# Kernel tuning notes

Measured on AMD Instinct MI355X. Metric: run time of the kernel, lower is better.

Reference implementation:

```python
import jax, jax.numpy as jnp
import numpy as np

BN_EPS = 1e-5
B, N, D, E, L, VOCAB = 256, 256, 256, 262144, 5, 16
V = B * N


def batch_norm(h, g, b):
    # BatchNorm1d in training mode: biased batch stats over the node axis
    mu = jnp.mean(h, axis=0)
    var = jnp.mean((h - mu) ** 2, axis=0)
    return (h - mu) * jax.lax.rsqrt(var + BN_EPS) * g + b


def setup_inputs() -> dict:
    key = jax.random.key(0)
    ks = jax.random.split(key, 10)
    return {
        "x": jax.random.normal(ks[0], (B, N + 1, D), jnp.float32),
        "edge_weight": jax.random.uniform(ks[1], (E,), jnp.float32),
        "bond_emb": 0.02 * jax.random.normal(ks[2], (L, 3, VOCAB, D), jnp.float32),
        "W1": 0.02 * jax.random.normal(ks[3], (L, D, 2 * D), jnp.float32),
        "b1": jnp.zeros((L, 2 * D), jnp.float32),
        "bn1_g": jnp.ones((L, 2 * D), jnp.float32),
        "bn1_b": jnp.zeros((L, 2 * D), jnp.float32),
        "W2": 0.02 * jax.random.normal(ks[4], (L, 2 * D, D), jnp.float32),
        "b2": jnp.zeros((L, D), jnp.float32),
        "bn2_g": jnp.ones((L, D), jnp.float32),
        "bn2_b": jnp.zeros((L, D), jnp.float32),
        "eps_param": jnp.zeros((L,), jnp.float32),
        "x_mask": jnp.ones((B, N), jnp.int32),
        "edge_index": jax.random.randint(ks[5], (2, E), 0, V, jnp.int32),
        "edge_attr": jax.random.randint(ks[6], (E, 3), 0, VOCAB, jnp.int32),
    }


def reference(x, edge_weight, bond_emb, W1, b1, bn1_g, bn1_b, W2, b2,
              bn2_g, bn2_b, eps_param, x_mask, edge_index, edge_attr):
    res = x
    # mask is all-ones -> x[x_mask] equals the flattened [B*N, D] node tensor
    h = x[:, 1:, :].reshape(-1, D)
    mask = x_mask.reshape(-1).astype(x.dtype)[:, None]

    # add_self_loops: append (i, i) for every node; self-loop attr = [5, 7, 0]
    sl = jnp.arange(V, dtype=edge_index.dtype)
    src = jnp.concatenate([edge_index[0], sl])
    dst = jnp.concatenate([edge_index[1], sl])
    ea = jnp.concatenate(
        [edge_attr, jnp.broadcast_to(jnp.array([5, 7, 0], edge_attr.dtype), (V, 3))], axis=0)
    ew = jnp.concatenate([edge_weight, jnp.ones((V,), edge_weight.dtype)])

    for i in range(L):
        # BondEncoder: sum of per-feature embedding lookups -> [E+V, D]
        eemb = (bond_emb[i, 0][ea[:, 0]] + bond_emb[i, 1][ea[:, 1]]
                + bond_emb[i, 2][ea[:, 2]])
        msg = jax.nn.relu(h[src] + eemb) * ew[:, None]       # gather + relu
        aggr = jax.ops.segment_sum(msg, dst, num_segments=V)  # scatter-add
        z = (1.0 + eps_param[i]) * h + aggr
        z = batch_norm(z @ W1[i] + b1[i], bn1_g[i], bn1_b[i])
        z = jax.nn.relu(z) @ W2[i] + b2[i]
        z = batch_norm(z, bn2_g[i], bn2_b[i])                 # GNNBlock norm
        if i != L - 1:                                        # last_act
            z = jax.nn.relu(z)
        h = z                                                  # drop_ratio=0

    rep = h * mask  # x_zeros[x_mask] = node_representation (JK='last')
    return res.at[:, 1:, :].add(rep.reshape(res.shape[0], -1, D))
```

## Files before the change

kernel.cpp:

```cpp
#include <hip/hip_runtime.h>

#define E_EDGES 262144
#define V_NODES 65536
#define D_DIM   256

typedef short bf16x8 __attribute__((ext_vector_type(8)));
typedef float f32x4  __attribute__((ext_vector_type(4)));

__device__ __forceinline__ unsigned short f2bf(float f) {
  union { float f; unsigned u; } x; x.f = f;
  unsigned r = x.u + 0x7FFFu + ((x.u >> 16) & 1u);
  return (unsigned short)(r >> 16);
}
__device__ __forceinline__ float bf2f(unsigned short h) {
  union { unsigned u; float f; } x; x.u = ((unsigned)h) << 16;
  return x.f;
}
__device__ __forceinline__ void async16(const void* g, void* l) {
  __builtin_amdgcn_global_load_lds(
      (const __attribute__((address_space(1))) unsigned*)g,
      (__attribute__((address_space(3))) unsigned*)l, 16, 0, 0);
}

__global__ __launch_bounds__(256) void convert_weights_kernel(
    const float* __restrict__ W1, const float* __restrict__ W2,
    unsigned short* __restrict__ W1T, unsigned short* __restrict__ W2T) {
  int idx = blockIdx.x * 256 + threadIdx.x;
  {
    int k = idx & 255, n = (idx >> 8) & 511, i = idx >> 17;
    W1T[idx] = f2bf(W1[((size_t)(i * 256 + k)) * 512 + n]);
  }
  {
    int k = idx & 511, n = (idx >> 9) & 255, i = idx >> 17;
    W2T[idx] = f2bf(W2[((size_t)(i * 512 + k)) * 256 + n]);
  }
}

__global__ void hist_kernel(const int* __restrict__ ei, int* __restrict__ counts) {
  int e = blockIdx.x * 256 + threadIdx.x;
  int d = (e < E_EDGES) ? ei[E_EDGES + e] : (e - E_EDGES);
  atomicAdd(&counts[d], 1);
}
__global__ void scan1_kernel(const int* __restrict__ counts, int* __restrict__ indptr,
                             int* __restrict__ bsums) {
  __shared__ int s[256];
  int t = threadIdx.x, b = blockIdx.x;
  int v = counts[b * 256 + t];
  s[t] = v; __syncthreads();
  for (int off = 1; off < 256; off <<= 1) {
    int add = (t >= off) ? s[t - off] : 0;
    __syncthreads();
    s[t] += add;
    __syncthreads();
  }
  indptr[b * 256 + t] = s[t] - v;
  if (t == 255) bsums[b] = s[255];
}
__global__ void scan2_kernel(const int* __restrict__ bsums, int* __restrict__ boff) {
  __shared__ int s[256];
  int t = threadIdx.x;
  int v = bsums[t];
  s[t] = v; __syncthreads();
  for (int off = 1; off < 256; off <<= 1) {
    int add = (t >= off) ? s[t - off] : 0;
    __syncthreads();
    s[t] += add;
    __syncthreads();
  }
  boff[t] = s[t] - v;
}
__global__ void scan3_kernel(int* __restrict__ indptr, const int* __restrict__ boff) {
  int t = threadIdx.x, b = blockIdx.x;
  indptr[b * 256 + t] += boff[b];
  if (b == 0 && t == 0) indptr[V_NODES] = E_EDGES + V_NODES;
}
__global__ void scatter_kernel(const int* __restrict__ ei, const int* __restrict__ indptr,
                               int* __restrict__ fill, int* __restrict__ csr_eid) {
  int e = blockIdx.x * 256 + threadIdx.x;
  int d = (e < E_EDGES) ? ei[E_EDGES + e] : (e - E_EDGES);
  int pos = indptr[d] + atomicAdd(&fill[d], 1);
  csr_eid[pos] = e;
}

template <bool L0>
__device__ __forceinline__ void load_hnorm(int node, int c0, const float* __restrict__ x,
                                           const unsigned short* __restrict__ hprev,
                                           const float* sc, const float* sh, float* out) {
  if (L0) {
    const float* p = x + ((size_t)((node >> 8) * 257 + (node & 255) + 1)) * 256 + c0;
    float4 tv = *(const float4*)p;
    out[0] = tv.x; out[1] = tv.y; out[2] = tv.z; out[3] = tv.w;
  } else {
    ushort4 tv = *(const ushort4*)(hprev + (size_t)node * 256 + c0);
    out[0] = fmaxf(bf2f(tv.x) * sc[0] + sh[0], 0.f);
    out[1] = fmaxf(bf2f(tv.y) * sc[1] + sh[1], 0.f);
    out[2] = fmaxf(bf2f(tv.z) * sc[2] + sh[2], 0.f);
    out[3] = fmaxf(bf2f(tv.w) * sc[3] + sh[3], 0.f);
  }
}

template <bool L0>
__global__ __launch_bounds__(256) void msg_kernel(
    const float* __restrict__ x, const unsigned short* __restrict__ hprev,
    const float* __restrict__ scale2, const float* __restrict__ shift2,
    const int* __restrict__ indptr, const int* __restrict__ csr_eid,
    const int* __restrict__ ei, const int* __restrict__ ea, const float* __restrict__ ew,
    const float* __restrict__ bemb, const float* __restrict__ eps_param, int layer,
    float* __restrict__ aggr_f) {
  int wid = threadIdx.x >> 6;
  int lane = threadIdx.x & 63;
  int v = blockIdx.x * 4 + wid;
  int c0 = lane * 4;
  float ep = 1.0f + eps_param[layer];

  float sc[4], sh[4];
  if (!L0) {
#pragma unroll
    for (int j = 0; j < 4; ++j) { sc[j] = scale2[c0 + j]; sh[j] = shift2[c0 + j]; }
  }

  float hv[4];
  load_hnorm<L0>(v, c0, x, hprev, sc, sh, hv);
  float acc[4] = { ep * hv[0], ep * hv[1], ep * hv[2], ep * hv[3] };

  int beg = indptr[v], end = indptr[v + 1];
  int eid = csr_eid[beg];
  int s, a0, a1, a2; float w;
  if (eid < E_EDGES) {
    s = ei[eid]; a0 = ea[eid * 3]; a1 = ea[eid * 3 + 1]; a2 = ea[eid * 3 + 2]; w = ew[eid];
  } else { s = eid - E_EDGES; a0 = 5; a1 = 7; a2 = 0; w = 1.0f; }

  for (int p = beg; p < end; ++p) {
    float hs[4];
    load_hnorm<L0>(s, c0, x, hprev, sc, sh, hs);
    float4 e0 = *(const float4*)(bemb + (size_t)(a0) * 256 + c0);
    float4 e1 = *(const float4*)(bemb + (size_t)(16 + a1) * 256 + c0);
    float4 e2 = *(const float4*)(bemb + (size_t)(32 + a2) * 256 + c0);
    float wc = w;

    if (p + 1 < end) {
      int eidn = csr_eid[p + 1];
      if (eidn < E_EDGES) {
        s = ei[eidn]; a0 = ea[eidn * 3]; a1 = ea[eidn * 3 + 1]; a2 = ea[eidn * 3 + 2];
        w = ew[eidn];
      } else { s = eidn - E_EDGES; a0 = 5; a1 = 7; a2 = 0; w = 1.0f; }
    }

    acc[0] += fmaxf(hs[0] + e0.x + e1.x + e2.x, 0.f) * wc;
    acc[1] += fmaxf(hs[1] + e0.y + e1.y + e2.y, 0.f) * wc;
    acc[2] += fmaxf(hs[2] + e0.z + e1.z + e2.z, 0.f) * wc;
    acc[3] += fmaxf(hs[3] + e0.w + e1.w + e2.w, 0.f) * wc;
  }
  float4 o; o.x = acc[0]; o.y = acc[1]; o.z = acc[2]; o.w = acc[3];
  *(float4*)(aggr_f + (size_t)v * 256 + c0) = o;
}

__global__ __launch_bounds__(256) void colsum_kernel(const float* __restrict__ aggr_f,
                                                     float* __restrict__ colsum) {
  int t = threadIdx.x;
  size_t base = (size_t)blockIdx.x * 64 * 256 + t;
  float s = 0.f;
#pragma unroll
  for (int r = 0; r < 64; ++r) s += aggr_f[base + (size_t)r * 256];
  atomicAdd(&colsum[t], s);
}

__global__ __launch_bounds__(256) void center_kernel(const float* __restrict__ aggr_f,
                                                     const float* __restrict__ colsum,
                                                     unsigned short* __restrict__ aggr_c) {
  size_t i = ((size_t)blockIdx.x * 256 + threadIdx.x) * 4;
  int c = (int)(i & 255);
  float4 v = *(const float4*)(aggr_f + i);
  const float inv = 1.0f / 65536.0f;
  ushort4 o;
  o.x = f2bf(v.x - colsum[c + 0] * inv);
  o.y = f2bf(v.y - colsum[c + 1] * inv);
  o.z = f2bf(v.z - colsum[c + 2] * inv);
  o.w = f2bf(v.w - colsum[c + 3] * inv);
  *(ushort4*)(aggr_c + i) = o;
}

template <int K, int N>
__global__ __launch_bounds__(256) void gemm_kernel(
    const unsigned short* __restrict__ A, const unsigned short* __restrict__ BT,
    const float* __restrict__ bias, unsigned short* __restrict__ C,
    float* __restrict__ sumP, float* __restrict__ sqP) {
  __shared__ char lds[16384];
  const int t = threadIdx.x;
  const int lane = t & 63;
  const int wid = t >> 6;
  const int waveM = wid >> 1, waveN = wid & 1;
  const int rowBase = blockIdx.x * 128;
  const int colBase = blockIdx.y * 128;
  const int kw = lane >> 4;
  const int l15 = lane & 15;

  f32x4 acc[4][4];
#pragma unroll
  for (int m = 0; m < 4; ++m)
#pragma unroll
    for (int n = 0; n < 4; ++n) acc[m][n] = (f32x4){0.f, 0.f, 0.f, 0.f};

  for (int k0 = 0; k0 < K; k0 += 32) {
#pragma unroll
    for (int c = 0; c < 2; ++c) {
      int row = c * 64 + (t >> 2);
      int gslot = (t & 3) ^ ((row >> 1) & 3);
      const unsigned short* ga = A + (size_t)(rowBase + row) * K + k0 + gslot * 8;
      async16(ga, lds + c * 4096 + wid * 1024);
      const unsigned short* gb = BT + (size_t)(colBase + row) * K + k0 + gslot * 8;
      async16(gb, lds + 8192 + c * 4096 + wid * 1024);
    }
    __syncthreads();

    bf16x8 af[4], bfr[4];
#pragma unroll
    for (int f = 0; f < 4; ++f) {
      int rA = waveM * 64 + f * 16 + l15;
      af[f] = *(const bf16x8*)(lds + rA * 64 + ((kw ^ ((rA >> 1) & 3)) * 16));
      int rB = waveN * 64 + f * 16 + l15;
      bfr[f] = *(const bf16x8*)(lds + 8192 + rB * 64 + ((kw ^ ((rB >> 1) & 3)) * 16));
    }
#pragma unroll
    for (int m = 0; m < 4; ++m)
#pragma unroll
      for (int n = 0; n < 4; ++n)
        acc[m][n] = __builtin_amdgcn_mfma_f32_16x16x32_bf16(af[m], bfr[n], acc[m][n], 0, 0, 0);
    __syncthreads();
  }

  const int cB = colBase + waveN * 64;
  const int rB0 = rowBase + waveM * 64;
#pragma unroll
  for (int n = 0; n < 4; ++n) {
    int col = cB + n * 16 + l15;
    float bcol = bias[col];
    float psum = 0.f, psq = 0.f;
#pragma unroll
    for (int m = 0; m < 4; ++m) {
#pragma unroll
      for (int r = 0; r < 4; ++r) {
        float val = acc[m][n][r] + bcol;
        int row = rB0 + m * 16 + kw * 4 + r;
        C[(size_t)row * N + col] = f2bf(val);
        psum += val; psq += val * val;
      }
    }
    psum += __shfl_xor(psum, 16); psum += __shfl_xor(psum, 32);
    psq  += __shfl_xor(psq, 16);  psq  += __shfl_xor(psq, 32);
    if (kw == 0) {
      int prow = blockIdx.x * 2 + waveM;
      sumP[(size_t)prow * N + col] = psum;
      sqP[(size_t)prow * N + col] = psq;
    }
  }
}

__global__ __launch_bounds__(256) void gemm2_kernel(
    const unsigned short* __restrict__ A , const unsigned short* __restrict__ BT,
    const float* __restrict__ scA, const float* __restrict__ shA,
    const float* __restrict__ bias, float* __restrict__ C ,
    float* __restrict__ sumP, float* __restrict__ sqP) {
  const int K = 512, N = 256;
  __shared__ char lds[16384];
  const int t = threadIdx.x;
  const int lane = t & 63;
  const int wid = t >> 6;
  const int waveM = wid >> 1, waveN = wid & 1;
  const int rowBase = blockIdx.x * 128;
  const int colBase = blockIdx.y * 128;
  const int kw = lane >> 4;
  const int l15 = lane & 15;

  f32x4 acc[4][4];
#pragma unroll
  for (int m = 0; m < 4; ++m)
#pragma unroll
    for (int n = 0; n < 4; ++n) acc[m][n] = (f32x4){0.f, 0.f, 0.f, 0.f};

  for (int k0 = 0; k0 < K; k0 += 32) {
#pragma unroll
    for (int c = 0; c < 2; ++c) {
      int row = c * 64 + (t >> 2);
      int gslot = (t & 3) ^ ((row >> 1) & 3);
      const unsigned short* gb = BT + (size_t)(colBase + row) * K + k0 + gslot * 8;
      async16(gb, lds + 8192 + c * 4096 + wid * 1024);
    }
#pragma unroll
    for (int c = 0; c < 2; ++c) {
      int row = c * 64 + (t >> 2);
      int gslot = (t & 3) ^ ((row >> 1) & 3);
      int kk = k0 + gslot * 8;
      const unsigned short* ga = A + (size_t)(rowBase + row) * K + kk;
      ushort4 a0 = *(const ushort4*)ga;
      ushort4 a1 = *(const ushort4*)(ga + 4);
      float4 s0 = *(const float4*)(scA + kk);
      float4 s1 = *(const float4*)(scA + kk + 4);
      float4 h0 = *(const float4*)(shA + kk);
      float4 h1 = *(const float4*)(shA + kk + 4);
      bf16x8 o;
      o[0] = (short)f2bf(fmaxf(bf2f(a0.x) * s0.x + h0.x, 0.f));
      o[1] = (short)f2bf(fmaxf(bf2f(a0.y) * s0.y + h0.y, 0.f));
      o[2] = (short)f2bf(fmaxf(bf2f(a0.z) * s0.z + h0.z, 0.f));
      o[3] = (short)f2bf(fmaxf(bf2f(a0.w) * s0.w + h0.w, 0.f));
      o[4] = (short)f2bf(fmaxf(bf2f(a1.x) * s1.x + h1.x, 0.f));
      o[5] = (short)f2bf(fmaxf(bf2f(a1.y) * s1.y + h1.y, 0.f));
      o[6] = (short)f2bf(fmaxf(bf2f(a1.z) * s1.z + h1.z, 0.f));
      o[7] = (short)f2bf(fmaxf(bf2f(a1.w) * s1.w + h1.w, 0.f));
      *(bf16x8*)(lds + c * 4096 + wid * 1024 + (t & 63) * 16) = o;
    }
    __syncthreads();

    bf16x8 af[4], bfr[4];
#pragma unroll
    for (int f = 0; f < 4; ++f) {
      int rA = waveM * 64 + f * 16 + l15;
      af[f] = *(const bf16x8*)(lds + rA * 64 + ((kw ^ ((rA >> 1) & 3)) * 16));
      int rB = waveN * 64 + f * 16 + l15;
      bfr[f] = *(const bf16x8*)(lds + 8192 + rB * 64 + ((kw ^ ((rB >> 1) & 3)) * 16));
    }
#pragma unroll
    for (int m = 0; m < 4; ++m)
#pragma unroll
      for (int n = 0; n < 4; ++n)
        acc[m][n] = __builtin_amdgcn_mfma_f32_16x16x32_bf16(af[m], bfr[n], acc[m][n], 0, 0, 0);
    __syncthreads();
  }

  const int cB = colBase + waveN * 64;
  const int rB0 = rowBase + waveM * 64;
#pragma unroll
  for (int n = 0; n < 4; ++n) {
    int col = cB + n * 16 + l15;
    float bcol = bias[col];
    float psum = 0.f, psq = 0.f;
#pragma unroll
    for (int m = 0; m < 4; ++m) {
#pragma unroll
      for (int r = 0; r < 4; ++r) {
        float val = acc[m][n][r] + bcol;
        int row = rB0 + m * 16 + kw * 4 + r;
        C[(size_t)row * N + col] = val;
        psum += val; psq += val * val;
      }
    }
    psum += __shfl_xor(psum, 16); psum += __shfl_xor(psum, 32);
    psq  += __shfl_xor(psq, 16);  psq  += __shfl_xor(psq, 32);
    if (kw == 0) {
      int prow = blockIdx.x * 2 + waveM;
      sumP[(size_t)prow * N + col] = psum;
      sqP[(size_t)prow * N + col] = psq;
    }
  }
}

__global__ void finalize_kernel(const float* __restrict__ sumP, const float* __restrict__ sqP,
                                const float* __restrict__ g, const float* __restrict__ b,
                                float* __restrict__ scale, float* __restrict__ shift, int N) {
  __shared__ float ls[256], lq[256];
  int col = blockIdx.x, t = threadIdx.x;
  float s = 0.f, q = 0.f;
  for (int r = t; r < 1024; r += 256) {
    s += sumP[(size_t)r * N + col];
    q += sqP[(size_t)r * N + col];
  }
  ls[t] = s; lq[t] = q; __syncthreads();
  for (int off = 128; off > 0; off >>= 1) {
    if (t < off) { ls[t] += ls[t + off]; lq[t] += lq[t + off]; }
    __syncthreads();
  }
  if (t == 0) {
    float inv = 1.0f / 65536.0f;
    float mu = ls[0] * inv;
    float var = lq[0] * inv - mu * mu;
    float sc = g[col] * rsqrtf(var + 1e-5f);
    scale[col] = sc;
    shift[col] = b[col] - mu * sc;
  }
}

__global__ void finalize2_kernel(const float* __restrict__ sumP, const float* __restrict__ sqP,
                                 const float* __restrict__ g, const float* __restrict__ b,
                                 float* __restrict__ scale, float* __restrict__ shift,
                                 float* __restrict__ mu_out, int N) {
  __shared__ float ls[256], lq[256];
  int col = blockIdx.x, t = threadIdx.x;
  float s = 0.f, q = 0.f;
  for (int r = t; r < 1024; r += 256) {
    s += sumP[(size_t)r * N + col];
    q += sqP[(size_t)r * N + col];
  }
  ls[t] = s; lq[t] = q; __syncthreads();
  for (int off = 128; off > 0; off >>= 1) {
    if (t < off) { ls[t] += ls[t + off]; lq[t] += lq[t + off]; }
    __syncthreads();
  }
  if (t == 0) {
    float inv = 1.0f / 65536.0f;
    float mu = ls[0] * inv;
    float var = lq[0] * inv - mu * mu;
    scale[col] = g[col] * rsqrtf(var + 1e-5f);
    shift[col] = b[col];
    mu_out[col] = mu;
  }
}

__global__ __launch_bounds__(256) void center2_kernel(const float* __restrict__ z2f,
                                                      const float* __restrict__ mu2,
                                                      unsigned short* __restrict__ z2c) {
  size_t i = ((size_t)blockIdx.x * 256 + threadIdx.x) * 4;
  int c = (int)(i & 255);
  float4 v = *(const float4*)(z2f + i);
  ushort4 o;
  o.x = f2bf(v.x - mu2[c + 0]);
  o.y = f2bf(v.y - mu2[c + 1]);
  o.z = f2bf(v.z - mu2[c + 2]);
  o.w = f2bf(v.w - mu2[c + 3]);
  *(ushort4*)(z2c + i) = o;
}

__global__ void final_out_kernel(const float* __restrict__ x, const unsigned short* __restrict__ z2c,
                                 const float* __restrict__ scale2, const float* __restrict__ shift2,
                                 const int* __restrict__ xmask, float* __restrict__ out) {
  int row = blockIdx.x;
  int b = blockIdx.y;
  int lane = threadIdx.x;
  size_t off = ((size_t)b * 257 + row) * 256 + lane * 4;
  float4 xv = *(const float4*)(x + off);
  if (row > 0) {
    int v = b * 256 + (row - 1);
    float m = (float)xmask[v];
    ushort4 tv = *(const ushort4*)(z2c + (size_t)v * 256 + lane * 4);
    int c = lane * 4;
    xv.x += m * (bf2f(tv.x) * scale2[c + 0] + shift2[c + 0]);
    xv.y += m * (bf2f(tv.y) * scale2[c + 1] + shift2[c + 1]);
    xv.z += m * (bf2f(tv.z) * scale2[c + 2] + shift2[c + 2]);
    xv.w += m * (bf2f(tv.w) * scale2[c + 3] + shift2[c + 3]);
  }
  *(float4*)(out + off) = xv;
}

extern "C" void kernel_launch(void* const* d_in, const int* in_sizes, int n_in,
                              void* d_out, int out_size, void* d_ws, size_t ws_size,
                              hipStream_t stream) {
  const float* x    = (const float*)d_in[0];
  const float* ew   = (const float*)d_in[1];
  const float* bemb = (const float*)d_in[2];
  const float* W1   = (const float*)d_in[3];
  const float* b1   = (const float*)d_in[4];
  const float* g1   = (const float*)d_in[5];
  const float* bb1  = (const float*)d_in[6];
  const float* W2   = (const float*)d_in[7];
  const float* b2   = (const float*)d_in[8];
  const float* g2   = (const float*)d_in[9];
  const float* bb2  = (const float*)d_in[10];
  const float* eps  = (const float*)d_in[11];
  const int* xmask  = (const int*)d_in[12];
  const int* ei     = (const int*)d_in[13];
  const int* ea     = (const int*)d_in[14];
  float* out = (float*)d_out;

  char* ws = (char*)d_ws;
  size_t off = 0;
  auto alloc = [&](size_t bytes) {
    char* p = ws + off;
    off += (bytes + 255) & ~(size_t)255;
    return p;
  };
  unsigned short* W1T = (unsigned short*)alloc(5ull * 512 * 256 * 2);
  unsigned short* W2T = (unsigned short*)alloc(5ull * 256 * 512 * 2);
  int* counts = (int*)alloc(65536ull * 4);
  int* fill   = (int*)alloc(65536ull * 4);
  int* indptr = (int*)alloc(65537ull * 4);
  int* bsums  = (int*)alloc(256 * 4);
  int* boff   = (int*)alloc(256 * 4);
  int* csr    = (int*)alloc(327680ull * 4);
  float* scale1 = (float*)alloc(512 * 4);
  float* shift1 = (float*)alloc(512 * 4);
  float* scale2 = (float*)alloc(256 * 4);
  float* shift2 = (float*)alloc(256 * 4);
  float* colsum = (float*)alloc(256 * 4);
  float* mu2    = (float*)alloc(256 * 4);
  float* sumP = (float*)alloc(1024ull * 512 * 4);
  float* sqP  = (float*)alloc(1024ull * 512 * 4);
  float* aggr_f = (float*)alloc(65536ull * 256 * 4);
  unsigned short* aggr_c = (unsigned short*)alloc(65536ull * 256 * 2);
  unsigned short* z1   = (unsigned short*)alloc(65536ull * 512 * 2);
  unsigned short* z2c  = (unsigned short*)alloc(65536ull * 256 * 2);
  (void)ws_size; (void)in_sizes; (void)n_in; (void)out_size;

  hipMemsetAsync(counts, 0, 65536ull * 4, stream);
  hipMemsetAsync(fill, 0, 65536ull * 4, stream);

  convert_weights_kernel<<<2560, 256, 0, stream>>>(W1, W2, W1T, W2T);
  hist_kernel<<<1280, 256, 0, stream>>>(ei, counts);
  scan1_kernel<<<256, 256, 0, stream>>>(counts, indptr, bsums);
  scan2_kernel<<<1, 256, 0, stream>>>(bsums, boff);
  scan3_kernel<<<256, 256, 0, stream>>>(indptr, boff);
  scatter_kernel<<<1280, 256, 0, stream>>>(ei, indptr, fill, csr);

  for (int i = 0; i < 5; ++i) {
    const float* bemb_l = bemb + (size_t)i * 3 * 16 * 256;
    if (i == 0)
      msg_kernel<true><<<16384, 256, 0, stream>>>(x, (const unsigned short*)nullptr, nullptr, nullptr,
                                                  indptr, csr, ei, ea, ew, bemb_l, eps, i, aggr_f);
    else
      msg_kernel<false><<<16384, 256, 0, stream>>>(x, z2c, scale2, shift2,
                                                   indptr, csr, ei, ea, ew, bemb_l, eps, i, aggr_f);
    hipMemsetAsync(colsum, 0, 256 * 4, stream);
    colsum_kernel<<<1024, 256, 0, stream>>>(aggr_f, colsum);
    center_kernel<<<16384, 256, 0, stream>>>(aggr_f, colsum, aggr_c);
    gemm_kernel<256, 512><<<dim3(512, 4), 256, 0, stream>>>(
        aggr_c, W1T + (size_t)i * 512 * 256, b1 + i * 512, z1, sumP, sqP);
    finalize_kernel<<<512, 256, 0, stream>>>(sumP, sqP, g1 + i * 512, bb1 + i * 512,
                                             scale1, shift1, 512);
    gemm2_kernel<<<dim3(512, 2), 256, 0, stream>>>(
        z1, W2T + (size_t)i * 256 * 512, scale1, shift1, b2 + i * 256, aggr_f, sumP, sqP);
    finalize2_kernel<<<256, 256, 0, stream>>>(sumP, sqP, g2 + i * 256, bb2 + i * 256,
                                              scale2, shift2, mu2, 256);
    center2_kernel<<<16384, 256, 0, stream>>>(aggr_f, mu2, z2c);
  }
  final_out_kernel<<<dim3(257, 256), 64, 0, stream>>>(x, z2c, scale2, shift2, xmask, out);
}
```

Measured before the change: 1.458 ms.

## Fuse centering into GEMM1 A-load, prefetch full edge data, skip last center2

The separate center kernel is removed. GEMM1 now reads fp32 aggregates directly, subtracts the column mean, converts to bf16 and writes the result into LDS, which avoids a full bf16 round trip through memory per layer. The message kernel now issues the next edge's feature and embedding loads one iteration ahead for deeper prefetch. The last layer also skips center2, and the final output is computed from the fp32 buffer. The cost is that GEMM1's A-tile path loses async global-to-LDS loads, so it reads twice the bytes and spends VALU work on the conversion.

```diff
diff --git a/kernel.cpp b/kernel.cpp
--- a/kernel.cpp
+++ b/kernel.cpp
@@ -83,20 +83,37 @@
 }
 
 template <bool L0>
-__device__ __forceinline__ void load_hnorm(int node, int c0, const float* __restrict__ x,
-                                           const unsigned short* __restrict__ hprev,
-                                           const float* sc, const float* sh, float* out) {
+struct EdgeBuf {
+  float4 hrawf;
+  ushort4 hrawb;
+  float4 e0, e1, e2;
+  float w;
+};
+
+template <bool L0>
+__device__ __forceinline__ void resolve_and_issue(
+    int p, int c0, const int* __restrict__ csr_eid, const int* __restrict__ ei,
+    const int* __restrict__ ea, const float* __restrict__ ew,
+    const float* __restrict__ x, const unsigned short* __restrict__ hprev,
+    const float* __restrict__ bemb, EdgeBuf<L0>& B) {
+  int eid = csr_eid[p];
+  int s, a0, a1, a2;
+  if (eid < E_EDGES) {
+    s = ei[eid];
+    a0 = ea[eid * 3]; a1 = ea[eid * 3 + 1]; a2 = ea[eid * 3 + 2];
+    B.w = ew[eid];
+  } else {
+    s = eid - E_EDGES; a0 = 5; a1 = 7; a2 = 0; B.w = 1.0f;
+  }
   if (L0) {
-    const float* p = x + ((size_t)((node >> 8) * 257 + (node & 255) + 1)) * 256 + c0;
-    float4 tv = *(const float4*)p;
-    out[0] = tv.x; out[1] = tv.y; out[2] = tv.z; out[3] = tv.w;
+    const float* pp = x + ((size_t)((s >> 8) * 257 + (s & 255) + 1)) * 256 + c0;
+    B.hrawf = *(const float4*)pp;
   } else {
-    ushort4 tv = *(const ushort4*)(hprev + (size_t)node * 256 + c0);
-    out[0] = fmaxf(bf2f(tv.x) * sc[0] + sh[0], 0.f);
-    out[1] = fmaxf(bf2f(tv.y) * sc[1] + sh[1], 0.f);
-    out[2] = fmaxf(bf2f(tv.z) * sc[2] + sh[2], 0.f);
-    out[3] = fmaxf(bf2f(tv.w) * sc[3] + sh[3], 0.f);
-  }
+    B.hrawb = *(const ushort4*)(hprev + (size_t)s * 256 + c0);
+  }
+  B.e0 = *(const float4*)(bemb + (size_t)(a0) * 256 + c0);
+  B.e1 = *(const float4*)(bemb + (size_t)(16 + a1) * 256 + c0);
+  B.e2 = *(const float4*)(bemb + (size_t)(32 + a2) * 256 + c0);
 }
 
 template <bool L0>
@@ -120,38 +137,49 @@
   }
 
   float hv[4];
-  load_hnorm<L0>(v, c0, x, hprev, sc, sh, hv);
-  float acc[4] = { ep * hv[0], ep * hv[1], ep * hv[2], ep * hv[3] };
+  if (L0) {
+    const float* p = x + ((size_t)((v >> 8) * 257 + (v & 255) + 1)) * 256 + c0;
+    float4 tv = *(const float4*)p;
+    hv[0] = tv.x; hv[1] = tv.y; hv[2] = tv.z; hv[3] = tv.w;
+  } else {
+    ushort4 tv = *(const ushort4*)(hprev + (size_t)v * 256 + c0);
+    hv[0] = fmaxf(bf2f(tv.x) * sc[0] + sh[0], 0.f);
+    hv[1] = fmaxf(bf2f(tv.y) * sc[1] + sh[1], 0.f);
+    hv[2] = fmaxf(bf2f(tv.z) * sc[2] + sh[2], 0.f);
+    hv[3] = fmaxf(bf2f(tv.w) * sc[3] + sh[3], 0.f);
+  }
+
+  float acc[4] = { 0.f, 0.f, 0.f, 0.f };
 
   int beg = indptr[v], end = indptr[v + 1];
-  int eid = csr_eid[beg];
-  int s, a0, a1, a2; float w;
-  if (eid < E_EDGES) {
-    s = ei[eid]; a0 = ea[eid * 3]; a1 = ea[eid * 3 + 1]; a2 = ea[eid * 3 + 2]; w = ew[eid];
-  } else { s = eid - E_EDGES; a0 = 5; a1 = 7; a2 = 0; w = 1.0f; }
+  EdgeBuf<L0> cur, nxt;
+  resolve_and_issue<L0>(beg, c0, csr_eid, ei, ea, ew, x, hprev, bemb, cur);
 
   for (int p = beg; p < end; ++p) {
+    if (p + 1 < end)
+      resolve_and_issue<L0>(p + 1, c0, csr_eid, ei, ea, ew, x, hprev, bemb, nxt);
+
     float hs[4];
-    load_hnorm<L0>(s, c0, x, hprev, sc, sh, hs);
-    float4 e0 = *(const float4*)(bemb + (size_t)(a0) * 256 + c0);
-    float4 e1 = *(const float4*)(bemb + (size_t)(16 + a1) * 256 + c0);
-    float4 e2 = *(const float4*)(bemb + (size_t)(32 + a2) * 256 + c0);
-    float wc = w;
-
-    if (p + 1 < end) {
-      int eidn = csr_eid[p + 1];
-      if (eidn < E_EDGES) {
-        s = ei[eidn]; a0 = ea[eidn * 3]; a1 = ea[eidn * 3 + 1]; a2 = ea[eidn * 3 + 2];
-        w = ew[eidn];
-      } else { s = eidn - E_EDGES; a0 = 5; a1 = 7; a2 = 0; w = 1.0f; }
-    }
-
-    acc[0] += fmaxf(hs[0] + e0.x + e1.x + e2.x, 0.f) * wc;
-    acc[1] += fmaxf(hs[1] + e0.y + e1.y + e2.y, 0.f) * wc;
-    acc[2] += fmaxf(hs[2] + e0.z + e1.z + e2.z, 0.f) * wc;
-    acc[3] += fmaxf(hs[3] + e0.w + e1.w + e2.w, 0.f) * wc;
-  }
-  float4 o; o.x = acc[0]; o.y = acc[1]; o.z = acc[2]; o.w = acc[3];
+    if (L0) {
+      hs[0] = cur.hrawf.x; hs[1] = cur.hrawf.y; hs[2] = cur.hrawf.z; hs[3] = cur.hrawf.w;
+    } else {
+      hs[0] = fmaxf(bf2f(cur.hrawb.x) * sc[0] + sh[0], 0.f);
+      hs[1] = fmaxf(bf2f(cur.hrawb.y) * sc[1] + sh[1], 0.f);
+      hs[2] = fmaxf(bf2f(cur.hrawb.z) * sc[2] + sh[2], 0.f);
+      hs[3] = fmaxf(bf2f(cur.hrawb.w) * sc[3] + sh[3], 0.f);
+    }
+    acc[0] += fmaxf(hs[0] + cur.e0.x + cur.e1.x + cur.e2.x, 0.f) * cur.w;
+    acc[1] += fmaxf(hs[1] + cur.e0.y + cur.e1.y + cur.e2.y, 0.f) * cur.w;
+    acc[2] += fmaxf(hs[2] + cur.e0.z + cur.e1.z + cur.e2.z, 0.f) * cur.w;
+    acc[3] += fmaxf(hs[3] + cur.e0.w + cur.e1.w + cur.e2.w, 0.f) * cur.w;
+    cur = nxt;
+  }
+
+  float4 o;
+  o.x = acc[0] + ep * hv[0];
+  o.y = acc[1] + ep * hv[1];
+  o.z = acc[2] + ep * hv[2];
+  o.w = acc[3] + ep * hv[3];
   *(float4*)(aggr_f + (size_t)v * 256 + c0) = o;
 }
 
@@ -165,26 +193,11 @@
   atomicAdd(&colsum[t], s);
 }
 
-__global__ __launch_bounds__(256) void center_kernel(const float* __restrict__ aggr_f,
-                                                     const float* __restrict__ colsum,
-                                                     unsigned short* __restrict__ aggr_c) {
-  size_t i = ((size_t)blockIdx.x * 256 + threadIdx.x) * 4;
-  int c = (int)(i & 255);
-  float4 v = *(const float4*)(aggr_f + i);
-  const float inv = 1.0f / 65536.0f;
-  ushort4 o;
-  o.x = f2bf(v.x - colsum[c + 0] * inv);
-  o.y = f2bf(v.y - colsum[c + 1] * inv);
-  o.z = f2bf(v.z - colsum[c + 2] * inv);
-  o.w = f2bf(v.w - colsum[c + 3] * inv);
-  *(ushort4*)(aggr_c + i) = o;
-}
-
-template <int K, int N>
-__global__ __launch_bounds__(256) void gemm_kernel(
-    const unsigned short* __restrict__ A, const unsigned short* __restrict__ BT,
-    const float* __restrict__ bias, unsigned short* __restrict__ C,
-    float* __restrict__ sumP, float* __restrict__ sqP) {
+__global__ __launch_bounds__(256) void gemm1_kernel(
+    const float* __restrict__ A , const unsigned short* __restrict__ BT,
+    const float* __restrict__ colsum, const float* __restrict__ bias,
+    unsigned short* __restrict__ C, float* __restrict__ sumP, float* __restrict__ sqP) {
+  const int K = 256, N = 512;
   __shared__ char lds[16384];
   const int t = threadIdx.x;
   const int lane = t & 63;
@@ -194,6 +207,7 @@
   const int colBase = blockIdx.y * 128;
   const int kw = lane >> 4;
   const int l15 = lane & 15;
+  const float inv = 1.0f / 65536.0f;
 
   f32x4 acc[4][4];
 #pragma unroll
@@ -206,10 +220,29 @@
     for (int c = 0; c < 2; ++c) {
       int row = c * 64 + (t >> 2);
       int gslot = (t & 3) ^ ((row >> 1) & 3);
-      const unsigned short* ga = A + (size_t)(rowBase + row) * K + k0 + gslot * 8;
-      async16(ga, lds + c * 4096 + wid * 1024);
       const unsigned short* gb = BT + (size_t)(colBase + row) * K + k0 + gslot * 8;
       async16(gb, lds + 8192 + c * 4096 + wid * 1024);
+    }
+#pragma unroll
+    for (int c = 0; c < 2; ++c) {
+      int row = c * 64 + (t >> 2);
+      int gslot = (t & 3) ^ ((row >> 1) & 3);
+      int kk = k0 + gslot * 8;
+      const float* ga = A + (size_t)(rowBase + row) * K + kk;
+      float4 a0 = *(const float4*)ga;
+      float4 a1 = *(const float4*)(ga + 4);
+      float4 m0 = *(const float4*)(colsum + kk);
+      float4 m1 = *(const float4*)(colsum + kk + 4);
+      bf16x8 o;
+      o[0] = (short)f2bf(a0.x - m0.x * inv);
+      o[1] = (short)f2bf(a0.y - m0.y * inv);
+      o[2] = (short)f2bf(a0.z - m0.z * inv);
+      o[3] = (short)f2bf(a0.w - m0.w * inv);
+      o[4] = (short)f2bf(a1.x - m1.x * inv);
+      o[5] = (short)f2bf(a1.y - m1.y * inv);
+      o[6] = (short)f2bf(a1.z - m1.z * inv);
+      o[7] = (short)f2bf(a1.w - m1.w * inv);
+      *(bf16x8*)(lds + c * 4096 + wid * 1024 + (t & 63) * 16) = o;
     }
     __syncthreads();
 
@@ -419,7 +452,8 @@
   *(ushort4*)(z2c + i) = o;
 }
 
-__global__ void final_out_kernel(const float* __restrict__ x, const unsigned short* __restrict__ z2c,
+__global__ void final_out_kernel(const float* __restrict__ x, const float* __restrict__ z2f,
+                                 const float* __restrict__ mu2,
                                  const float* __restrict__ scale2, const float* __restrict__ shift2,
                                  const int* __restrict__ xmask, float* __restrict__ out) {
   int row = blockIdx.x;
@@ -430,12 +464,12 @@
   if (row > 0) {
     int v = b * 256 + (row - 1);
     float m = (float)xmask[v];
-    ushort4 tv = *(const ushort4*)(z2c + (size_t)v * 256 + lane * 4);
+    float4 tv = *(const float4*)(z2f + (size_t)v * 256 + lane * 4);
     int c = lane * 4;
-    xv.x += m * (bf2f(tv.x) * scale2[c + 0] + shift2[c + 0]);
-    xv.y += m * (bf2f(tv.y) * scale2[c + 1] + shift2[c + 1]);
-    xv.z += m * (bf2f(tv.z) * scale2[c + 2] + shift2[c + 2]);
-    xv.w += m * (bf2f(tv.w) * scale2[c + 3] + shift2[c + 3]);
+    xv.x += m * ((tv.x - mu2[c + 0]) * scale2[c + 0] + shift2[c + 0]);
+    xv.y += m * ((tv.y - mu2[c + 1]) * scale2[c + 1] + shift2[c + 1]);
+    xv.z += m * ((tv.z - mu2[c + 2]) * scale2[c + 2] + shift2[c + 2]);
+    xv.w += m * ((tv.w - mu2[c + 3]) * scale2[c + 3] + shift2[c + 3]);
   }
   *(float4*)(out + off) = xv;
 }
@@ -484,7 +518,6 @@
   float* sumP = (float*)alloc(1024ull * 512 * 4);
   float* sqP  = (float*)alloc(1024ull * 512 * 4);
   float* aggr_f = (float*)alloc(65536ull * 256 * 4);
-  unsigned short* aggr_c = (unsigned short*)alloc(65536ull * 256 * 2);
   unsigned short* z1   = (unsigned short*)alloc(65536ull * 512 * 2);
   unsigned short* z2c  = (unsigned short*)alloc(65536ull * 256 * 2);
   (void)ws_size; (void)in_sizes; (void)n_in; (void)out_size;
@@ -509,16 +542,16 @@
                                                    indptr, csr, ei, ea, ew, bemb_l, eps, i, aggr_f);
     hipMemsetAsync(colsum, 0, 256 * 4, stream);
     colsum_kernel<<<1024, 256, 0, stream>>>(aggr_f, colsum);
-    center_kernel<<<16384, 256, 0, stream>>>(aggr_f, colsum, aggr_c);
-    gemm_kernel<256, 512><<<dim3(512, 4), 256, 0, stream>>>(
-        aggr_c, W1T + (size_t)i * 512 * 256, b1 + i * 512, z1, sumP, sqP);
+    gemm1_kernel<<<dim3(512, 4), 256, 0, stream>>>(
+        aggr_f, W1T + (size_t)i * 512 * 256, colsum, b1 + i * 512, z1, sumP, sqP);
     finalize_kernel<<<512, 256, 0, stream>>>(sumP, sqP, g1 + i * 512, bb1 + i * 512,
                                              scale1, shift1, 512);
     gemm2_kernel<<<dim3(512, 2), 256, 0, stream>>>(
         z1, W2T + (size_t)i * 256 * 512, scale1, shift1, b2 + i * 256, aggr_f, sumP, sqP);
     finalize2_kernel<<<256, 256, 0, stream>>>(sumP, sqP, g2 + i * 256, bb2 + i * 256,
                                               scale2, shift2, mu2, 256);
-    center2_kernel<<<16384, 256, 0, stream>>>(aggr_f, mu2, z2c);
-  }
-  final_out_kernel<<<dim3(257, 256), 64, 0, stream>>>(x, z2c, scale2, shift2, xmask, out);
-}
+    if (i != 4)
+      center2_kernel<<<16384, 256, 0, stream>>>(aggr_f, mu2, z2c);
+  }
+  final_out_kernel<<<dim3(257, 256), 64, 0, stream>>>(x, aggr_f, mu2, scale2, shift2, xmask, out);
+}
```

After: 1.445 ms. Within noise of the previous version (-0.9%).
